# Kernel tuning notes

Hardware: AMD Instinct MI355X
Metric: run time of the kernel (lower is better)

Reference implementation:

```python
import jax, jax.numpy as jnp
import numpy as np

N_NODES = 50000
N_EDGES = 800000
IN_FEATS = 96
HIDDEN = 48


def setup_inputs() -> dict:
    key = jax.random.key(0)
    ks = jax.random.split(key, 16)
    x = jax.random.normal(ks[0], (N_NODES, IN_FEATS), dtype=jnp.float32)
    edge_index = jax.random.randint(ks[1], (2, N_EDGES), 0, N_NODES, dtype=jnp.int32)

    def lin(k, fan_in, fan_out):
        s = 1.0 / np.sqrt(fan_in)
        return jax.random.uniform(k, (fan_in, fan_out), jnp.float32, -s, s)

    return {
        "x": x,
        "edge_index": edge_index,
        # SAGEConv layer 0: in -> hidden
        "w_self0": lin(ks[2], IN_FEATS, HIDDEN),
        "w_neigh0": lin(ks[3], IN_FEATS, HIDDEN),
        "b0": jnp.zeros((HIDDEN,), jnp.float32),
        # SAGEConv layer 1: hidden -> hidden
        "w_self1": lin(ks[4], HIDDEN, HIDDEN),
        "w_neigh1": lin(ks[5], HIDDEN, HIDDEN),
        "b1": jnp.zeros((HIDDEN,), jnp.float32),
        # SAGEConv layer 2: hidden -> hidden
        "w_self2": lin(ks[6], HIDDEN, HIDDEN),
        "w_neigh2": lin(ks[7], HIDDEN, HIDDEN),
        "b2": jnp.zeros((HIDDEN,), jnp.float32),
        # prediction head: hidden -> 1
        "w_pred": lin(ks[8], HIDDEN, 1),
        "b_pred": jnp.zeros((1,), jnp.float32),
    }


def _sage_mean(x, src, dst, deg_inv, w_self, w_neigh, b):
    # mean over in-neighbors: gather src features, segment-sum at dst, / in-degree
    agg = jax.ops.segment_sum(x[src], dst, num_segments=N_NODES) * deg_inv  # [N, F]
    return x @ w_self + agg @ w_neigh + b


def reference(x, edge_index, w_self0, w_neigh0, b0, w_self1, w_neigh1, b1,
              w_self2, w_neigh2, b2, w_pred, b_pred):
    src, dst = edge_index[0], edge_index[1]
    deg = jax.ops.segment_sum(jnp.ones((src.shape[0],), x.dtype), dst,
                              num_segments=N_NODES)
    deg_inv = (1.0 / jnp.maximum(deg, 1.0))[:, None]  # isolated nodes -> 0 agg

    h = jax.nn.relu(_sage_mean(x, src, dst, deg_inv, w_self0, w_neigh0, b0))
    h = jax.nn.relu(_sage_mean(h, src, dst, deg_inv, w_self1, w_neigh1, b1))
    h = jax.nn.relu(_sage_mean(h, src, dst, deg_inv, w_self2, w_neigh2, b2))
    return h @ w_pred + b_pred  # [N, 1]
```

## Files before the change

kernel.cpp:

```cpp
#include <hip/hip_runtime.h>


constexpr int HID = 48;
constexpr int MAXDEG = 64;
constexpr int GNB = 64;

__global__ __launch_bounds__(128) void fill_proj_k(
    const float* __restrict__ X, const float* __restrict__ Wn,
    const float* __restrict__ Ws, const float* __restrict__ bias,
    float* __restrict__ p_out, float* __restrict__ s_out, int n_nodes,
    const int* __restrict__ src, const int* __restrict__ dst,
    int* __restrict__ cnt, unsigned short* __restrict__ buckets,
    int n_edges, int gemm_blocks) {
    __shared__ float wlds[96 * HID];
    __shared__ float bias_lds[HID];
    const int t = threadIdx.x;

    if ((int)blockIdx.x >= gemm_blocks) {
        int base = (blockIdx.x - gemm_blocks) * 256 + t;
        int e0 = base, e1 = base + 128;
        if (e0 < n_edges) {
            int d = dst[e0];
            int s = src[e0];
            int pos = atomicAdd(&cnt[d], 1);
            if (pos < MAXDEG) buckets[(size_t)d * MAXDEG + pos] = (unsigned short)s;
        }
        if (e1 < n_edges) {
            int d = dst[e1];
            int s = src[e1];
            int pos = atomicAdd(&cnt[d], 1);
            if (pos < MAXDEG) buckets[(size_t)d * MAXDEG + pos] = (unsigned short)s;
        }
        return;
    }

    const int q = t & 3;
    const int m = t >> 2;
    const int jb = q * 12;
    const int n0 = blockIdx.x * GNB + 2 * m;
    const int n1 = n0 + 1;
    const bool v0 = n0 < n_nodes, v1 = n1 < n_nodes;
    const int cn0 = v0 ? n0 : 0, cn1 = v1 ? n1 : 0;
    const float4* xr0 = reinterpret_cast<const float4*>(X + (size_t)cn0 * 96);
    const float4* xr1 = reinterpret_cast<const float4*>(X + (size_t)cn1 * 96);

    for (int i = t; i < 96 * HID; i += 128) wlds[i] = Wn[i];
    __syncthreads();
    {
        float pa[12], pb[12];
#pragma unroll
        for (int j = 0; j < 12; ++j) { pa[j] = 0.0f; pb[j] = 0.0f; }
#pragma unroll 4
        for (int k4 = 0; k4 < 24; ++k4) {
            float4 xa = xr0[k4];
            float4 xb = xr1[k4];
#pragma unroll
            for (int c = 0; c < 4; ++c) {
                float x0 = (c == 0) ? xa.x : (c == 1) ? xa.y : (c == 2) ? xa.z : xa.w;
                float x1 = (c == 0) ? xb.x : (c == 1) ? xb.y : (c == 2) ? xb.z : xb.w;
                const float4* wr =
                    reinterpret_cast<const float4*>(&wlds[(k4 * 4 + c) * HID + jb]);
#pragma unroll
                for (int j4 = 0; j4 < 3; ++j4) {
                    float4 wv = wr[j4];
                    pa[j4 * 4 + 0] = fmaf(x0, wv.x, pa[j4 * 4 + 0]);
                    pa[j4 * 4 + 1] = fmaf(x0, wv.y, pa[j4 * 4 + 1]);
                    pa[j4 * 4 + 2] = fmaf(x0, wv.z, pa[j4 * 4 + 2]);
                    pa[j4 * 4 + 3] = fmaf(x0, wv.w, pa[j4 * 4 + 3]);
                    pb[j4 * 4 + 0] = fmaf(x1, wv.x, pb[j4 * 4 + 0]);
                    pb[j4 * 4 + 1] = fmaf(x1, wv.y, pb[j4 * 4 + 1]);
                    pb[j4 * 4 + 2] = fmaf(x1, wv.z, pb[j4 * 4 + 2]);
                    pb[j4 * 4 + 3] = fmaf(x1, wv.w, pb[j4 * 4 + 3]);
                }
            }
        }
        float4* po0 = reinterpret_cast<float4*>(p_out + (size_t)n0 * HID + jb);
        float4* po1 = reinterpret_cast<float4*>(p_out + (size_t)n1 * HID + jb);
#pragma unroll
        for (int j4 = 0; j4 < 3; ++j4) {
            if (v0) po0[j4] = make_float4(pa[j4 * 4 + 0], pa[j4 * 4 + 1],
                                          pa[j4 * 4 + 2], pa[j4 * 4 + 3]);
            if (v1) po1[j4] = make_float4(pb[j4 * 4 + 0], pb[j4 * 4 + 1],
                                          pb[j4 * 4 + 2], pb[j4 * 4 + 3]);
        }
    }
    __syncthreads();

    for (int i = t; i < 96 * HID; i += 128) wlds[i] = Ws[i];
    if (t < HID) bias_lds[t] = bias[t];
    __syncthreads();
    {
        float sa[12], sb[12];
#pragma unroll
        for (int j = 0; j < 12; ++j) {
            float b = bias_lds[jb + j];
            sa[j] = b; sb[j] = b;
        }
#pragma unroll 4
        for (int k4 = 0; k4 < 24; ++k4) {
            float4 xa = xr0[k4];
            float4 xb = xr1[k4];
#pragma unroll
            for (int c = 0; c < 4; ++c) {
                float x0 = (c == 0) ? xa.x : (c == 1) ? xa.y : (c == 2) ? xa.z : xa.w;
                float x1 = (c == 0) ? xb.x : (c == 1) ? xb.y : (c == 2) ? xb.z : xb.w;
                const float4* wr =
                    reinterpret_cast<const float4*>(&wlds[(k4 * 4 + c) * HID + jb]);
#pragma unroll
                for (int j4 = 0; j4 < 3; ++j4) {
                    float4 wv = wr[j4];
                    sa[j4 * 4 + 0] = fmaf(x0, wv.x, sa[j4 * 4 + 0]);
                    sa[j4 * 4 + 1] = fmaf(x0, wv.y, sa[j4 * 4 + 1]);
                    sa[j4 * 4 + 2] = fmaf(x0, wv.z, sa[j4 * 4 + 2]);
                    sa[j4 * 4 + 3] = fmaf(x0, wv.w, sa[j4 * 4 + 3]);
                    sb[j4 * 4 + 0] = fmaf(x1, wv.x, sb[j4 * 4 + 0]);
                    sb[j4 * 4 + 1] = fmaf(x1, wv.y, sb[j4 * 4 + 1]);
                    sb[j4 * 4 + 2] = fmaf(x1, wv.z, sb[j4 * 4 + 2]);
                    sb[j4 * 4 + 3] = fmaf(x1, wv.w, sb[j4 * 4 + 3]);
                }
            }
        }
        float4* so0 = reinterpret_cast<float4*>(s_out + (size_t)n0 * HID + jb);
        float4* so1 = reinterpret_cast<float4*>(s_out + (size_t)n1 * HID + jb);
#pragma unroll
        for (int j4 = 0; j4 < 3; ++j4) {
            if (v0) so0[j4] = make_float4(sa[j4 * 4 + 0], sa[j4 * 4 + 1],
                                          sa[j4 * 4 + 2], sa[j4 * 4 + 3]);
            if (v1) so1[j4] = make_float4(sb[j4 * 4 + 0], sb[j4 * 4 + 1],
                                          sb[j4 * 4 + 2], sb[j4 * 4 + 3]);
        }
    }
}

template <bool LAST>
__global__ __launch_bounds__(128, 4) void fused_layer_k(
    const float* __restrict__ p_in, const float* __restrict__ s_in,
    const int* __restrict__ cnt, const unsigned short* __restrict__ buckets,
    const float* __restrict__ wn_next, const float* __restrict__ ws_next,
    const float* __restrict__ b_next, const float* __restrict__ w_pred,
    const float* __restrict__ b_pred, float* __restrict__ p_out,
    float* __restrict__ s_out, float* __restrict__ out, int n_nodes) {
    __shared__ float wn_lds[LAST ? 4 : HID * HID];
    __shared__ float ws_lds[LAST ? 4 : HID * HID];
    __shared__ float bn_lds[HID];
    __shared__ float wp_lds[HID];

    const int t = threadIdx.x;
    if (!LAST) {
        for (int i = t; i < HID * HID; i += 128) {
            wn_lds[i] = wn_next[i];
            ws_lds[i] = ws_next[i];
        }
        if (t < HID) bn_lds[t] = b_next[t];
    } else {
        if (t < HID) wp_lds[t] = w_pred[t];
    }
    __syncthreads();

    const int q = t & 3;
    const int e = (t >> 2) & 1;
    const int m = t >> 3;
    const int n = blockIdx.x * 16 + m;
    if (n >= n_nodes) return;
    const int jb = q * 12;

    const int deg = min(cnt[n], MAXDEG);
    const float di = 1.0f / fmaxf((float)deg, 1.0f);
    const unsigned short* bkt = buckets + (size_t)n * MAXDEG;

    float4 ga[3], gb[3];
#pragma unroll
    for (int c = 0; c < 3; ++c) {
        ga[c] = make_float4(0.f, 0.f, 0.f, 0.f);
        gb[c] = make_float4(0.f, 0.f, 0.f, 0.f);
    }
    int i = e;
    for (; i + 2 < deg; i += 4) {
        int s0 = bkt[i], s1 = bkt[i + 2];
        const float4* r0 = reinterpret_cast<const float4*>(p_in + (size_t)s0 * HID + jb);
        const float4* r1 = reinterpret_cast<const float4*>(p_in + (size_t)s1 * HID + jb);
#pragma unroll
        for (int c = 0; c < 3; ++c) {
            float4 a = r0[c], b = r1[c];
            ga[c].x += a.x; ga[c].y += a.y; ga[c].z += a.z; ga[c].w += a.w;
            gb[c].x += b.x; gb[c].y += b.y; gb[c].z += b.z; gb[c].w += b.w;
        }
    }
    if (i < deg) {
        int s0 = bkt[i];
        const float4* r0 = reinterpret_cast<const float4*>(p_in + (size_t)s0 * HID + jb);
#pragma unroll
        for (int c = 0; c < 3; ++c) {
            float4 a = r0[c];
            ga[c].x += a.x; ga[c].y += a.y; ga[c].z += a.z; ga[c].w += a.w;
        }
    }
    float g[12];
#pragma unroll
    for (int c = 0; c < 3; ++c) {
        g[c * 4 + 0] = ga[c].x + gb[c].x;
        g[c * 4 + 1] = ga[c].y + gb[c].y;
        g[c * 4 + 2] = ga[c].z + gb[c].z;
        g[c * 4 + 3] = ga[c].w + gb[c].w;
    }
#pragma unroll
    for (int j = 0; j < 12; ++j) g[j] += __shfl_xor(g[j], 4, 64);

    const float4* sr = reinterpret_cast<const float4*>(s_in + (size_t)n * HID + jb);
    float h[12];
#pragma unroll
    for (int j4 = 0; j4 < 3; ++j4) {
        float4 sv = sr[j4];
        h[j4 * 4 + 0] = fmaxf(fmaf(di, g[j4 * 4 + 0], sv.x), 0.0f);
        h[j4 * 4 + 1] = fmaxf(fmaf(di, g[j4 * 4 + 1], sv.y), 0.0f);
        h[j4 * 4 + 2] = fmaxf(fmaf(di, g[j4 * 4 + 2], sv.z), 0.0f);
        h[j4 * 4 + 3] = fmaxf(fmaf(di, g[j4 * 4 + 3], sv.w), 0.0f);
    }

    if (LAST) {
        float s = 0.0f;
#pragma unroll
        for (int j = 0; j < 12; ++j) s = fmaf(h[j], wp_lds[jb + j], s);
        s += __shfl_xor(s, 1, 64);
        s += __shfl_xor(s, 2, 64);
        if ((t & 7) == 0) out[n] = s + b_pred[0];
        return;
    }

    float pa[12], sa[12];
#pragma unroll
    for (int j = 0; j < 12; ++j) {
        pa[j] = 0.0f;
        sa[j] = (e == 0) ? bn_lds[jb + j] : 0.0f;
    }
    const int kb = e * 24;
#pragma unroll
    for (int kk = 0; kk < 24; ++kk) {
        const int k = kb + kk;
        const int srcl = (t & ~3) | (k / 12);
        float hs = __shfl(h[kk % 12], srcl, 64);
        const float4* wnr = reinterpret_cast<const float4*>(&wn_lds[k * HID + jb]);
        const float4* wsr = reinterpret_cast<const float4*>(&ws_lds[k * HID + jb]);
#pragma unroll
        for (int j4 = 0; j4 < 3; ++j4) {
            float4 wv = wnr[j4];
            pa[j4 * 4 + 0] = fmaf(hs, wv.x, pa[j4 * 4 + 0]);
            pa[j4 * 4 + 1] = fmaf(hs, wv.y, pa[j4 * 4 + 1]);
            pa[j4 * 4 + 2] = fmaf(hs, wv.z, pa[j4 * 4 + 2]);
            pa[j4 * 4 + 3] = fmaf(hs, wv.w, pa[j4 * 4 + 3]);
            float4 uv = wsr[j4];
            sa[j4 * 4 + 0] = fmaf(hs, uv.x, sa[j4 * 4 + 0]);
            sa[j4 * 4 + 1] = fmaf(hs, uv.y, sa[j4 * 4 + 1]);
            sa[j4 * 4 + 2] = fmaf(hs, uv.z, sa[j4 * 4 + 2]);
            sa[j4 * 4 + 3] = fmaf(hs, uv.w, sa[j4 * 4 + 3]);
        }
    }
#pragma unroll
    for (int j = 0; j < 12; ++j) {
        pa[j] += __shfl_xor(pa[j], 4, 64);
        sa[j] += __shfl_xor(sa[j], 4, 64);
    }
    if (e == 0) {
        float4* po = reinterpret_cast<float4*>(p_out + (size_t)n * HID + jb);
#pragma unroll
        for (int j4 = 0; j4 < 3; ++j4)
            po[j4] = make_float4(pa[j4 * 4 + 0], pa[j4 * 4 + 1],
                                 pa[j4 * 4 + 2], pa[j4 * 4 + 3]);
    } else {
        float4* so = reinterpret_cast<float4*>(s_out + (size_t)n * HID + jb);
#pragma unroll
        for (int j4 = 0; j4 < 3; ++j4)
            so[j4] = make_float4(sa[j4 * 4 + 0], sa[j4 * 4 + 1],
                                 sa[j4 * 4 + 2], sa[j4 * 4 + 3]);
    }
}

extern "C" void kernel_launch(void* const* d_in, const int* in_sizes, int n_in,
                              void* d_out, int out_size, void* d_ws, size_t ws_size,
                              hipStream_t stream) {
    const float* x        = (const float*)d_in[0];
    const int*   ei       = (const int*)d_in[1];
    const float* w_self0  = (const float*)d_in[2];
    const float* w_neigh0 = (const float*)d_in[3];
    const float* b0       = (const float*)d_in[4];
    const float* w_self1  = (const float*)d_in[5];
    const float* w_neigh1 = (const float*)d_in[6];
    const float* b1       = (const float*)d_in[7];
    const float* w_self2  = (const float*)d_in[8];
    const float* w_neigh2 = (const float*)d_in[9];
    const float* b2       = (const float*)d_in[10];
    const float* w_pred   = (const float*)d_in[11];
    const float* b_pred   = (const float*)d_in[12];

    const int n_nodes = in_sizes[0] / 96;
    const int n_edges = in_sizes[1] / 2;
    const int* src = ei;
    const int* dst = ei + n_edges;

    char* wsb = (char*)d_ws;
    int* cnt                = (int*)wsb;              wsb += (size_t)n_nodes * 4;
    unsigned short* buckets = (unsigned short*)wsb;   wsb += (size_t)n_nodes * MAXDEG * 2;
    float* pA = (float*)wsb;                          wsb += (size_t)n_nodes * HID * 4;
    float* sA = (float*)wsb;                          wsb += (size_t)n_nodes * HID * 4;
    float* pB = (float*)wsb;                          wsb += (size_t)n_nodes * HID * 4;
    float* sB = (float*)wsb;                          wsb += (size_t)n_nodes * HID * 4;
    float* out = (float*)d_out;

    const int gnb = (n_nodes + GNB - 1) / GNB;
    const int fb = (n_edges + 255) / 256;
    const int lb = (n_nodes + 15) / 16;

    hipMemsetAsync(cnt, 0, (size_t)n_nodes * 4, stream);

    fill_proj_k<<<gnb + fb, 128, 0, stream>>>(x, w_neigh0, w_self0, b0, pA, sA,
                                              n_nodes, src, dst, cnt, buckets,
                                              n_edges, gnb);
    fused_layer_k<false><<<lb, 128, 0, stream>>>(pA, sA, cnt, buckets,
                                                 w_neigh1, w_self1, b1,
                                                 nullptr, nullptr, pB, sB,
                                                 nullptr, n_nodes);
    fused_layer_k<false><<<lb, 128, 0, stream>>>(pB, sB, cnt, buckets,
                                                 w_neigh2, w_self2, b2,
                                                 nullptr, nullptr, pA, sA,
                                                 nullptr, n_nodes);
    fused_layer_k<true><<<lb, 128, 0, stream>>>(pA, sA, cnt, buckets,
                                                nullptr, nullptr, nullptr,
                                                w_pred, b_pred, nullptr,
                                                nullptr, out, n_nodes);
}
```

Baseline: 246.8 us.

## Store intermediate features in fp16 and aggregate-then-project for later layers

Gathered feature rows (the layer-0 neighbour projection and the hidden activations) are now stored as fp16 rather than fp32, which halves the bytes read in the random-access neighbour gathers. The later layers are restructured to aggregate raw activations first and then apply both weight matrices in one kernel. This stores only the fp16 activation per node instead of separate neighbour and self projections. The first layer's output is split into its own activation kernel. fp16 storage reduces accuracy and could affect tolerance checks.

Result: faster. 219.2 us (-11.2%).

```diff
diff --git a/kernel.cpp b/kernel.cpp
--- a/kernel.cpp
+++ b/kernel.cpp
@@ -1,14 +1,59 @@
 #include <hip/hip_runtime.h>
+#include <hip/hip_fp16.h>
 
 
 constexpr int HID = 48;
 constexpr int MAXDEG = 64;
 constexpr int GNB = 64;
 
+__device__ __forceinline__ unsigned pack_h2(float a, float b) {
+    __half2 h = __floats2half2_rn(a, b);
+    return *reinterpret_cast<unsigned*>(&h);
+}
+__device__ __forceinline__ void acc_u2(float* g, uint2 u) {
+    __half2 h0 = *reinterpret_cast<__half2*>(&u.x);
+    __half2 h1 = *reinterpret_cast<__half2*>(&u.y);
+    float2 f0 = __half22float2(h0), f1 = __half22float2(h1);
+    g[0] += f0.x; g[1] += f0.y; g[2] += f1.x; g[3] += f1.y;
+}
+__device__ __forceinline__ void unpack_u2(float* v, uint2 u) {
+    __half2 h0 = *reinterpret_cast<__half2*>(&u.x);
+    __half2 h1 = *reinterpret_cast<__half2*>(&u.y);
+    float2 f0 = __half22float2(h0), f1 = __half22float2(h1);
+    v[0] = f0.x; v[1] = f0.y; v[2] = f1.x; v[3] = f1.y;
+}
+
+__device__ __forceinline__ void gather_h(const __half* __restrict__ p,
+                                         const unsigned short* __restrict__ bkt,
+                                         int deg, int e, int jb, float* g) {
+    float ga[12], gb[12];
+#pragma unroll
+    for (int j = 0; j < 12; ++j) { ga[j] = 0.0f; gb[j] = 0.0f; }
+    int i = e;
+    for (; i + 2 < deg; i += 4) {
+        int s0 = bkt[i], s1 = bkt[i + 2];
+        const uint2* r0 = reinterpret_cast<const uint2*>(p + (size_t)s0 * HID + jb);
+        const uint2* r1 = reinterpret_cast<const uint2*>(p + (size_t)s1 * HID + jb);
+        uint2 a0 = r0[0], a1 = r0[1], a2 = r0[2];
+        uint2 b0 = r1[0], b1 = r1[1], b2 = r1[2];
+        acc_u2(ga + 0, a0); acc_u2(ga + 4, a1); acc_u2(ga + 8, a2);
+        acc_u2(gb + 0, b0); acc_u2(gb + 4, b1); acc_u2(gb + 8, b2);
+    }
+    if (i < deg) {
+        const uint2* r0 = reinterpret_cast<const uint2*>(p + (size_t)bkt[i] * HID + jb);
+        uint2 a0 = r0[0], a1 = r0[1], a2 = r0[2];
+        acc_u2(ga + 0, a0); acc_u2(ga + 4, a1); acc_u2(ga + 8, a2);
+    }
+#pragma unroll
+    for (int j = 0; j < 12; ++j) g[j] = ga[j] + gb[j];
+#pragma unroll
+    for (int j = 0; j < 12; ++j) g[j] += __shfl_xor(g[j], 4, 64);
+}
+
 __global__ __launch_bounds__(128) void fill_proj_k(
     const float* __restrict__ X, const float* __restrict__ Wn,
     const float* __restrict__ Ws, const float* __restrict__ bias,
-    float* __restrict__ p_out, float* __restrict__ s_out, int n_nodes,
+    __half* __restrict__ p_out, float* __restrict__ s_out, int n_nodes,
     const int* __restrict__ src, const int* __restrict__ dst,
     int* __restrict__ cnt, unsigned short* __restrict__ buckets,
     int n_edges, int gemm_blocks) {
@@ -74,14 +119,17 @@
                 }
             }
         }
-        float4* po0 = reinterpret_cast<float4*>(p_out + (size_t)n0 * HID + jb);
-        float4* po1 = reinterpret_cast<float4*>(p_out + (size_t)n1 * HID + jb);
-#pragma unroll
-        for (int j4 = 0; j4 < 3; ++j4) {
-            if (v0) po0[j4] = make_float4(pa[j4 * 4 + 0], pa[j4 * 4 + 1],
-                                          pa[j4 * 4 + 2], pa[j4 * 4 + 3]);
-            if (v1) po1[j4] = make_float4(pb[j4 * 4 + 0], pb[j4 * 4 + 1],
-                                          pb[j4 * 4 + 2], pb[j4 * 4 + 3]);
+        if (v0) {
+            uint2* po = reinterpret_cast<uint2*>(p_out + (size_t)n0 * HID + jb);
+            po[0] = make_uint2(pack_h2(pa[0], pa[1]), pack_h2(pa[2], pa[3]));
+            po[1] = make_uint2(pack_h2(pa[4], pa[5]), pack_h2(pa[6], pa[7]));
+            po[2] = make_uint2(pack_h2(pa[8], pa[9]), pack_h2(pa[10], pa[11]));
+        }
+        if (v1) {
+            uint2* po = reinterpret_cast<uint2*>(p_out + (size_t)n1 * HID + jb);
+            po[0] = make_uint2(pack_h2(pb[0], pb[1]), pack_h2(pb[2], pb[3]));
+            po[1] = make_uint2(pack_h2(pb[4], pb[5]), pack_h2(pb[6], pb[7]));
+            po[2] = make_uint2(pack_h2(pb[8], pb[9]), pack_h2(pb[10], pb[11]));
         }
     }
     __syncthreads();
@@ -132,31 +180,11 @@
     }
 }
 
-template <bool LAST>
-__global__ __launch_bounds__(128, 4) void fused_layer_k(
-    const float* __restrict__ p_in, const float* __restrict__ s_in,
+__global__ __launch_bounds__(128, 8) void act_k(
+    const __half* __restrict__ p_in, const float* __restrict__ s_in,
     const int* __restrict__ cnt, const unsigned short* __restrict__ buckets,
-    const float* __restrict__ wn_next, const float* __restrict__ ws_next,
-    const float* __restrict__ b_next, const float* __restrict__ w_pred,
-    const float* __restrict__ b_pred, float* __restrict__ p_out,
-    float* __restrict__ s_out, float* __restrict__ out, int n_nodes) {
-    __shared__ float wn_lds[LAST ? 4 : HID * HID];
-    __shared__ float ws_lds[LAST ? 4 : HID * HID];
-    __shared__ float bn_lds[HID];
-    __shared__ float wp_lds[HID];
-
+    __half* __restrict__ h_out, int n_nodes) {
     const int t = threadIdx.x;
-    if (!LAST) {
-        for (int i = t; i < HID * HID; i += 128) {
-            wn_lds[i] = wn_next[i];
-            ws_lds[i] = ws_next[i];
-        }
-        if (t < HID) bn_lds[t] = b_next[t];
-    } else {
-        if (t < HID) wp_lds[t] = w_pred[t];
-    }
-    __syncthreads();
-
     const int q = t & 3;
     const int e = (t >> 2) & 1;
     const int m = t >> 3;
@@ -166,112 +194,117 @@
 
     const int deg = min(cnt[n], MAXDEG);
     const float di = 1.0f / fmaxf((float)deg, 1.0f);
-    const unsigned short* bkt = buckets + (size_t)n * MAXDEG;
-
-    float4 ga[3], gb[3];
-#pragma unroll
-    for (int c = 0; c < 3; ++c) {
-        ga[c] = make_float4(0.f, 0.f, 0.f, 0.f);
-        gb[c] = make_float4(0.f, 0.f, 0.f, 0.f);
-    }
-    int i = e;
-    for (; i + 2 < deg; i += 4) {
-        int s0 = bkt[i], s1 = bkt[i + 2];
-        const float4* r0 = reinterpret_cast<const float4*>(p_in + (size_t)s0 * HID + jb);
-        const float4* r1 = reinterpret_cast<const float4*>(p_in + (size_t)s1 * HID + jb);
-#pragma unroll
-        for (int c = 0; c < 3; ++c) {
-            float4 a = r0[c], b = r1[c];
-            ga[c].x += a.x; ga[c].y += a.y; ga[c].z += a.z; ga[c].w += a.w;
-            gb[c].x += b.x; gb[c].y += b.y; gb[c].z += b.z; gb[c].w += b.w;
-        }
-    }
-    if (i < deg) {
-        int s0 = bkt[i];
-        const float4* r0 = reinterpret_cast<const float4*>(p_in + (size_t)s0 * HID + jb);
-#pragma unroll
-        for (int c = 0; c < 3; ++c) {
-            float4 a = r0[c];
-            ga[c].x += a.x; ga[c].y += a.y; ga[c].z += a.z; ga[c].w += a.w;
-        }
-    }
     float g[12];
-#pragma unroll
-    for (int c = 0; c < 3; ++c) {
-        g[c * 4 + 0] = ga[c].x + gb[c].x;
-        g[c * 4 + 1] = ga[c].y + gb[c].y;
-        g[c * 4 + 2] = ga[c].z + gb[c].z;
-        g[c * 4 + 3] = ga[c].w + gb[c].w;
-    }
-#pragma unroll
-    for (int j = 0; j < 12; ++j) g[j] += __shfl_xor(g[j], 4, 64);
-
-    const float4* sr = reinterpret_cast<const float4*>(s_in + (size_t)n * HID + jb);
-    float h[12];
-#pragma unroll
-    for (int j4 = 0; j4 < 3; ++j4) {
-        float4 sv = sr[j4];
-        h[j4 * 4 + 0] = fmaxf(fmaf(di, g[j4 * 4 + 0], sv.x), 0.0f);
-        h[j4 * 4 + 1] = fmaxf(fmaf(di, g[j4 * 4 + 1], sv.y), 0.0f);
-        h[j4 * 4 + 2] = fmaxf(fmaf(di, g[j4 * 4 + 2], sv.z), 0.0f);
-        h[j4 * 4 + 3] = fmaxf(fmaf(di, g[j4 * 4 + 3], sv.w), 0.0f);
-    }
+    gather_h(p_in, buckets + (size_t)n * MAXDEG, deg, e, jb, g);
+
+    if (e == 0) {
+        const float4* sr = reinterpret_cast<const float4*>(s_in + (size_t)n * HID + jb);
+        float h[12];
+#pragma unroll
+        for (int j4 = 0; j4 < 3; ++j4) {
+            float4 sv = sr[j4];
+            h[j4 * 4 + 0] = fmaxf(fmaf(di, g[j4 * 4 + 0], sv.x), 0.0f);
+            h[j4 * 4 + 1] = fmaxf(fmaf(di, g[j4 * 4 + 1], sv.y), 0.0f);
+            h[j4 * 4 + 2] = fmaxf(fmaf(di, g[j4 * 4 + 2], sv.z), 0.0f);
+            h[j4 * 4 + 3] = fmaxf(fmaf(di, g[j4 * 4 + 3], sv.w), 0.0f);
+        }
+        uint2* ho = reinterpret_cast<uint2*>(h_out + (size_t)n * HID + jb);
+        ho[0] = make_uint2(pack_h2(h[0], h[1]), pack_h2(h[2], h[3]));
+        ho[1] = make_uint2(pack_h2(h[4], h[5]), pack_h2(h[6], h[7]));
+        ho[2] = make_uint2(pack_h2(h[8], h[9]), pack_h2(h[10], h[11]));
+    }
+}
+
+template <bool LAST>
+__global__ __launch_bounds__(128, 4) void layer_k(
+    const __half* __restrict__ h_in, const int* __restrict__ cnt,
+    const unsigned short* __restrict__ buckets, const float* __restrict__ wn,
+    const float* __restrict__ ws, const float* __restrict__ bn,
+    const float* __restrict__ w_pred, const float* __restrict__ b_pred,
+    __half* __restrict__ h_out, float* __restrict__ out, int n_nodes) {
+    __shared__ float wn_lds[HID * HID];
+    __shared__ float ws_lds[HID * HID];
+    __shared__ float bn_lds[HID];
+    __shared__ float wp_lds[HID];
+
+    const int t = threadIdx.x;
+    for (int i = t; i < HID * HID; i += 128) {
+        wn_lds[i] = wn[i];
+        ws_lds[i] = ws[i];
+    }
+    if (t < HID) bn_lds[t] = bn[t];
+    if (LAST && t < HID) wp_lds[t] = w_pred[t];
+    __syncthreads();
+
+    const int q = t & 3;
+    const int e = (t >> 2) & 1;
+    const int m = t >> 3;
+    const int n = blockIdx.x * 16 + m;
+    if (n >= n_nodes) return;
+    const int jb = q * 12;
+
+    const int deg = min(cnt[n], MAXDEG);
+    const float di = 1.0f / fmaxf((float)deg, 1.0f);
+    float g[12];
+    gather_h(h_in, buckets + (size_t)n * MAXDEG, deg, e, jb, g);
+#pragma unroll
+    for (int j = 0; j < 12; ++j) g[j] *= di;
+
+    float hs_own[12];
+    {
+        const uint2* hr = reinterpret_cast<const uint2*>(h_in + (size_t)n * HID + jb);
+        uint2 a = hr[0], b = hr[1], c = hr[2];
+        unpack_u2(hs_own + 0, a); unpack_u2(hs_own + 4, b); unpack_u2(hs_own + 8, c);
+    }
+
+    float acc[12];
+#pragma unroll
+    for (int j = 0; j < 12; ++j) acc[j] = (e == 0) ? bn_lds[jb + j] : 0.0f;
+
+    const int kb = e * 24;
+#pragma unroll
+    for (int kk = 0; kk < 24; ++kk) {
+        const int k = kb + kk;
+        const int srcl = (t & ~3) | (k / 12);
+        float gs = __shfl(g[kk % 12], srcl, 64);
+        float hv = __shfl(hs_own[kk % 12], srcl, 64);
+        const float4* wnr = reinterpret_cast<const float4*>(&wn_lds[k * HID + jb]);
+        const float4* wsr = reinterpret_cast<const float4*>(&ws_lds[k * HID + jb]);
+#pragma unroll
+        for (int j4 = 0; j4 < 3; ++j4) {
+            float4 wv = wnr[j4];
+            acc[j4 * 4 + 0] = fmaf(gs, wv.x, acc[j4 * 4 + 0]);
+            acc[j4 * 4 + 1] = fmaf(gs, wv.y, acc[j4 * 4 + 1]);
+            acc[j4 * 4 + 2] = fmaf(gs, wv.z, acc[j4 * 4 + 2]);
+            acc[j4 * 4 + 3] = fmaf(gs, wv.w, acc[j4 * 4 + 3]);
+            float4 uv = wsr[j4];
+            acc[j4 * 4 + 0] = fmaf(hv, uv.x, acc[j4 * 4 + 0]);
+            acc[j4 * 4 + 1] = fmaf(hv, uv.y, acc[j4 * 4 + 1]);
+            acc[j4 * 4 + 2] = fmaf(hv, uv.z, acc[j4 * 4 + 2]);
+            acc[j4 * 4 + 3] = fmaf(hv, uv.w, acc[j4 * 4 + 3]);
+        }
+    }
+#pragma unroll
+    for (int j = 0; j < 12; ++j) acc[j] += __shfl_xor(acc[j], 4, 64);
 
     if (LAST) {
         float s = 0.0f;
 #pragma unroll
-        for (int j = 0; j < 12; ++j) s = fmaf(h[j], wp_lds[jb + j], s);
+        for (int j = 0; j < 12; ++j) s = fmaf(fmaxf(acc[j], 0.0f), wp_lds[jb + j], s);
         s += __shfl_xor(s, 1, 64);
         s += __shfl_xor(s, 2, 64);
         if ((t & 7) == 0) out[n] = s + b_pred[0];
         return;
     }
 
-    float pa[12], sa[12];
-#pragma unroll
-    for (int j = 0; j < 12; ++j) {
-        pa[j] = 0.0f;
-        sa[j] = (e == 0) ? bn_lds[jb + j] : 0.0f;
-    }
-    const int kb = e * 24;
-#pragma unroll
-    for (int kk = 0; kk < 24; ++kk) {
-        const int k = kb + kk;
-        const int srcl = (t & ~3) | (k / 12);
-        float hs = __shfl(h[kk % 12], srcl, 64);
-        const float4* wnr = reinterpret_cast<const float4*>(&wn_lds[k * HID + jb]);
-        const float4* wsr = reinterpret_cast<const float4*>(&ws_lds[k * HID + jb]);
-#pragma unroll
-        for (int j4 = 0; j4 < 3; ++j4) {
-            float4 wv = wnr[j4];
-            pa[j4 * 4 + 0] = fmaf(hs, wv.x, pa[j4 * 4 + 0]);
-            pa[j4 * 4 + 1] = fmaf(hs, wv.y, pa[j4 * 4 + 1]);
-            pa[j4 * 4 + 2] = fmaf(hs, wv.z, pa[j4 * 4 + 2]);
-            pa[j4 * 4 + 3] = fmaf(hs, wv.w, pa[j4 * 4 + 3]);
-            float4 uv = wsr[j4];
-            sa[j4 * 4 + 0] = fmaf(hs, uv.x, sa[j4 * 4 + 0]);
-            sa[j4 * 4 + 1] = fmaf(hs, uv.y, sa[j4 * 4 + 1]);
-            sa[j4 * 4 + 2] = fmaf(hs, uv.z, sa[j4 * 4 + 2]);
-            sa[j4 * 4 + 3] = fmaf(hs, uv.w, sa[j4 * 4 + 3]);
-        }
-    }
-#pragma unroll
-    for (int j = 0; j < 12; ++j) {
-        pa[j] += __shfl_xor(pa[j], 4, 64);
-        sa[j] += __shfl_xor(sa[j], 4, 64);
-    }
     if (e == 0) {
-        float4* po = reinterpret_cast<float4*>(p_out + (size_t)n * HID + jb);
-#pragma unroll
-        for (int j4 = 0; j4 < 3; ++j4)
-            po[j4] = make_float4(pa[j4 * 4 + 0], pa[j4 * 4 + 1],
-                                 pa[j4 * 4 + 2], pa[j4 * 4 + 3]);
-    } else {
-        float4* so = reinterpret_cast<float4*>(s_out + (size_t)n * HID + jb);
-#pragma unroll
-        for (int j4 = 0; j4 < 3; ++j4)
-            so[j4] = make_float4(sa[j4 * 4 + 0], sa[j4 * 4 + 1],
-                                 sa[j4 * 4 + 2], sa[j4 * 4 + 3]);
+        float h[12];
+#pragma unroll
+        for (int j = 0; j < 12; ++j) h[j] = fmaxf(acc[j], 0.0f);
+        uint2* ho = reinterpret_cast<uint2*>(h_out + (size_t)n * HID + jb);
+        ho[0] = make_uint2(pack_h2(h[0], h[1]), pack_h2(h[2], h[3]));
+        ho[1] = make_uint2(pack_h2(h[4], h[5]), pack_h2(h[6], h[7]));
+        ho[2] = make_uint2(pack_h2(h[8], h[9]), pack_h2(h[10], h[11]));
     }
 }
 
@@ -300,10 +333,10 @@
     char* wsb = (char*)d_ws;
     int* cnt                = (int*)wsb;              wsb += (size_t)n_nodes * 4;
     unsigned short* buckets = (unsigned short*)wsb;   wsb += (size_t)n_nodes * MAXDEG * 2;
-    float* pA = (float*)wsb;                          wsb += (size_t)n_nodes * HID * 4;
-    float* sA = (float*)wsb;                          wsb += (size_t)n_nodes * HID * 4;
-    float* pB = (float*)wsb;                          wsb += (size_t)n_nodes * HID * 4;
-    float* sB = (float*)wsb;                          wsb += (size_t)n_nodes * HID * 4;
+    __half* p0 = (__half*)wsb;                        wsb += (size_t)n_nodes * HID * 2;
+    __half* h1 = (__half*)wsb;                        wsb += (size_t)n_nodes * HID * 2;
+    __half* h2 = (__half*)wsb;                        wsb += (size_t)n_nodes * HID * 2;
+    float* s0 = (float*)wsb;                          wsb += (size_t)n_nodes * HID * 4;
     float* out = (float*)d_out;
 
     const int gnb = (n_nodes + GNB - 1) / GNB;
@@ -312,19 +345,14 @@
 
     hipMemsetAsync(cnt, 0, (size_t)n_nodes * 4, stream);
 
-    fill_proj_k<<<gnb + fb, 128, 0, stream>>>(x, w_neigh0, w_self0, b0, pA, sA,
+    fill_proj_k<<<gnb + fb, 128, 0, stream>>>(x, w_neigh0, w_self0, b0, p0, s0,
                                               n_nodes, src, dst, cnt, buckets,
                                               n_edges, gnb);
-    fused_layer_k<false><<<lb, 128, 0, stream>>>(pA, sA, cnt, buckets,
-                                                 w_neigh1, w_self1, b1,
-                                                 nullptr, nullptr, pB, sB,
-                                                 nullptr, n_nodes);
-    fused_layer_k<false><<<lb, 128, 0, stream>>>(pB, sB, cnt, buckets,
-                                                 w_neigh2, w_self2, b2,
-                                                 nullptr, nullptr, pA, sA,
-                                                 nullptr, n_nodes);
-    fused_layer_k<true><<<lb, 128, 0, stream>>>(pA, sA, cnt, buckets,
-                                                nullptr, nullptr, nullptr,
-                                                w_pred, b_pred, nullptr,
-                                                nullptr, out, n_nodes);
-}
+    act_k<<<lb, 128, 0, stream>>>(p0, s0, cnt, buckets, h1, n_nodes);
+    layer_k<false><<<lb, 128, 0, stream>>>(h1, cnt, buckets, w_neigh1, w_self1,
+                                           b1, nullptr, nullptr, h2, nullptr,
+                                           n_nodes);
+    layer_k<true><<<lb, 128, 0, stream>>>(h2, cnt, buckets, w_neigh2, w_self2,
+                                          b2, w_pred, b_pred, nullptr, out,
+                                          n_nodes);
+}
```
